# Kernel tuning notes

Measured on AMD Instinct MI355X. Metric: run time of the kernel, lower is better.

## Reference

```python
import jax, jax.numpy as jnp
import numpy as np

D_MODEL, H, D_K, D_V = 512, 8, 64, 64
S_Q, S_KV = 2048, 2048


def setup_inputs() -> dict:
    key = jax.random.key(0)
    ks = jax.random.split(key, 11)
    sc = 0.02
    return {
        "embeddings": jax.random.normal(ks[0], (S_Q, D_MODEL), jnp.float32),
        "K": jax.random.normal(ks[1], (S_KV, D_MODEL), jnp.float32),
        "V": jax.random.normal(ks[2], (S_KV, D_MODEL), jnp.float32),
        # per-head projection weights (stacked over heads) + biases
        "Wq": jax.random.normal(ks[3], (H, D_MODEL, D_K), jnp.float32) * sc,
        "bq": jax.random.normal(ks[4], (H, D_K), jnp.float32) * sc,
        "Wk": jax.random.normal(ks[5], (H, D_MODEL, D_K), jnp.float32) * sc,
        "bk": jax.random.normal(ks[6], (H, D_K), jnp.float32) * sc,
        "Wv": jax.random.normal(ks[7], (H, D_MODEL, D_V), jnp.float32) * sc,
        "bv": jax.random.normal(ks[8], (H, D_V), jnp.float32) * sc,
        # final linear: [h*d_v -> d_model]
        "Wo": jax.random.normal(ks[9], (H * D_V, D_MODEL), jnp.float32) * sc,
        "bo": jax.random.normal(ks[10], (D_MODEL,), jnp.float32) * sc,
    }


def reference(embeddings, K, V, Wq, bq, Wk, bk, Wv, bv, Wo, bo):
    # Batched per-head projections (the original loops over h heads; math identical)
    q = jnp.einsum("sd,hdk->hsk", embeddings, Wq) + bq[:, None, :]  # [h, Sq, d_k]
    k = jnp.einsum("td,hdk->htk", K, Wk) + bk[:, None, :]           # [h, Skv, d_k]
    v = jnp.einsum("td,hdv->htv", V, Wv) + bv[:, None, :]           # [h, Skv, d_v]
    scores = jnp.einsum("hsk,htk->hst", q, k) / jnp.sqrt(jnp.asarray(D_K, q.dtype))
    attn = jax.nn.softmax(scores, axis=-1)                           # [h, Sq, Skv]
    out = jnp.einsum("hst,htv->hsv", attn, v)                        # [h, Sq, d_v]
    # torch.cat(results, dim=1): head 0's d_v columns first -> [Sq, h*d_v]
    concat = jnp.transpose(out, (1, 0, 2)).reshape(S_Q, H * D_V)
    return concat @ Wo + bo                                          # [Sq, d_model]
```

## Files before the change

### kernel.cpp

```cpp
#include <hip/hip_runtime.h>

#define SQ 2048
#define DM 512
#define NH 8
#define NSPLIT 4

typedef __bf16 bf16x8 __attribute__((ext_vector_type(8)));
typedef float f32x4 __attribute__((ext_vector_type(4)));
typedef unsigned short us8 __attribute__((ext_vector_type(8)));

__device__ __forceinline__ unsigned short f2bf(float f) {
    unsigned u = __builtin_bit_cast(unsigned, f);
    u += 0x7fffu + ((u >> 16) & 1u);
    return (unsigned short)(u >> 16);
}
__device__ __forceinline__ float bf2f(unsigned short u) {
    return __builtin_bit_cast(float, (unsigned)u << 16);
}

__global__ __launch_bounds__(256) void convert_all(
    const float* __restrict__ emb, const float* __restrict__ Kin, const float* __restrict__ Vin,
    const float* __restrict__ Wq,  const float* __restrict__ Wk,  const float* __restrict__ Wv,
    const float* __restrict__ Wo,
    unsigned short* __restrict__ xe, unsigned short* __restrict__ xk, unsigned short* __restrict__ xv,
    unsigned short* __restrict__ Wt,
    unsigned short* __restrict__ Woth, unsigned short* __restrict__ Wotl)
{
    const int b = blockIdx.x, tid = threadIdx.x;
    __shared__ float ld[64 * 68];
    float4* ld4 = reinterpret_cast<float4*>(ld);

    if (b < 1536) {
        const int m = b >> 9;
        const float* src = (m == 0) ? emb : (m == 1) ? Kin : Vin;
        unsigned short* dst = (m == 0) ? xe : (m == 1) ? xk : xv;
        const int oct = (b & 511) * 256 + tid;
        const float4* s4 = reinterpret_cast<const float4*>(src + (size_t)oct * 8);
        float4 f0 = s4[0], f1 = s4[1];
        us8 o;
        o[0] = f2bf(f0.x); o[1] = f2bf(f0.y); o[2] = f2bf(f0.z); o[3] = f2bf(f0.w);
        o[4] = f2bf(f1.x); o[5] = f2bf(f1.y); o[6] = f2bf(f1.z); o[7] = f2bf(f1.w);
        *reinterpret_cast<us8*>(dst + (size_t)oct * 8) = o;
    } else if (b < 1728) {
        const int wi = b - 1536;
        const int idx = wi >> 3;
        const int kt = wi & 7;
        const int p = idx >> 3, h = idx & 7;
        const float* src = ((p == 0) ? Wq : (p == 1) ? Wk : Wv)
                         + (size_t)h * 512 * 64 + (size_t)kt * 64 * 64;
        unsigned short* dst = Wt + (size_t)idx * 64 * 512 + kt * 64;
        const int rr = tid >> 4, c4 = tid & 15;
        #pragma unroll
        for (int it = 0; it < 4; it++) {
            int r = rr + 16 * it;
            ld4[r * 17 + c4] = reinterpret_cast<const float4*>(src + (size_t)r * 64)[c4];
        }
        __syncthreads();
        #pragma unroll
        for (int it = 0; it < 2; it++) {
            int slot = tid + it * 256;
            int n = slot >> 3, g = slot & 7;
            us8 o;
            #pragma unroll
            for (int i = 0; i < 8; i++)
                o[i] = f2bf(ld[(g * 8 + i) * 68 + n]);
            *reinterpret_cast<us8*>(dst + (size_t)n * 512 + g * 8) = o;
        }
    } else {
        const int ti = b - 1728;
        const int kt = ti >> 3, nt = ti & 7;
        const float* src = Wo + (size_t)kt * 64 * 512 + nt * 64;
        const int rr = tid >> 4, c4 = tid & 15;
        #pragma unroll
        for (int it = 0; it < 4; it++) {
            int r = rr + 16 * it;
            ld4[r * 17 + c4] = reinterpret_cast<const float4*>(src + (size_t)r * 512)[c4];
        }
        __syncthreads();
        #pragma unroll
        for (int it = 0; it < 2; it++) {
            int slot = tid + it * 256;
            int n = slot >> 3, g = slot & 7;
            us8 oh, ol;
            #pragma unroll
            for (int i = 0; i < 8; i++) {
                float v = ld[(g * 8 + i) * 68 + n];
                unsigned short hi = f2bf(v);
                oh[i] = hi;
                ol[i] = f2bf(v - bf2f(hi));
            }
            size_t doff = (size_t)(nt * 64 + n) * 512 + kt * 64 + g * 8;
            *reinterpret_cast<us8*>(Woth + doff) = oh;
            *reinterpret_cast<us8*>(Wotl + doff) = ol;
        }
    }
}

__global__ __launch_bounds__(256) void qkv_mfma(
    const unsigned short* __restrict__ xe, const unsigned short* __restrict__ xk,
    const unsigned short* __restrict__ xv, const unsigned short* __restrict__ Wt,
    const float* __restrict__ bq, const float* __restrict__ bk, const float* __restrict__ bv,
    unsigned short* __restrict__ qo, unsigned short* __restrict__ ko, unsigned short* __restrict__ vo)
{
    const int p = blockIdx.z, h = blockIdx.y, s0 = blockIdx.x * 64;
    const unsigned short* X = (p == 0) ? xe : (p == 1) ? xk : xv;
    const unsigned short* W = Wt + (size_t)(p * 8 + h) * 64 * 512;
    const float* B = ((p == 0) ? bq : (p == 1) ? bk : bv) + h * 64;

    const int tid = threadIdx.x;
    const int w = tid >> 6, lane = tid & 63, cl = lane & 15, q4 = lane >> 4;
    const int sr = tid >> 3, sg = tid & 7;

    __shared__ unsigned short As[2][64 * 72];
    __shared__ unsigned short Bs[2][64 * 72];

    #pragma unroll
    for (int it = 0; it < 2; it++) {
        int r = sr + 32 * it;
        *reinterpret_cast<float4*>(&As[0][r * 72 + sg * 8]) =
            *reinterpret_cast<const float4*>(&X[(size_t)(s0 + r) * 512 + sg * 8]);
        *reinterpret_cast<float4*>(&Bs[0][r * 72 + sg * 8]) =
            *reinterpret_cast<const float4*>(&W[(size_t)r * 512 + sg * 8]);
    }

    f32x4 acc[4] = {};

    for (int c = 0; c < 8; c++) {
        __syncthreads();
        const int buf = c & 1;
        const bool more = (c + 1 < 8);
        float4 ar[2], br[2];
        if (more) {
            #pragma unroll
            for (int it = 0; it < 2; it++) {
                int r = sr + 32 * it;
                ar[it] = *reinterpret_cast<const float4*>(
                    &X[(size_t)(s0 + r) * 512 + (c + 1) * 64 + sg * 8]);
                br[it] = *reinterpret_cast<const float4*>(
                    &W[(size_t)r * 512 + (c + 1) * 64 + sg * 8]);
            }
        }

        bf16x8 a0 = *reinterpret_cast<const bf16x8*>(&As[buf][(16 * w + cl) * 72 + q4 * 8]);
        bf16x8 a1 = *reinterpret_cast<const bf16x8*>(&As[buf][(16 * w + cl) * 72 + 32 + q4 * 8]);
        #pragma unroll
        for (int nn = 0; nn < 4; nn++) {
            bf16x8 b0 = *reinterpret_cast<const bf16x8*>(&Bs[buf][(16 * nn + cl) * 72 + q4 * 8]);
            bf16x8 b1 = *reinterpret_cast<const bf16x8*>(&Bs[buf][(16 * nn + cl) * 72 + 32 + q4 * 8]);
            acc[nn] = __builtin_amdgcn_mfma_f32_16x16x32_bf16(a0, b0, acc[nn], 0, 0, 0);
            acc[nn] = __builtin_amdgcn_mfma_f32_16x16x32_bf16(a1, b1, acc[nn], 0, 0, 0);
        }

        if (more) {
            const int nbuf = buf ^ 1;
            #pragma unroll
            for (int it = 0; it < 2; it++) {
                int r = sr + 32 * it;
                *reinterpret_cast<float4*>(&As[nbuf][r * 72 + sg * 8]) = ar[it];
                *reinterpret_cast<float4*>(&Bs[nbuf][r * 72 + sg * 8]) = br[it];
            }
        }
    }

    if (p == 0) {
        #pragma unroll
        for (int nn = 0; nn < 4; nn++) {
            int col = 16 * nn + cl;
            float bb = B[col];
            #pragma unroll
            for (int r = 0; r < 4; r++)
                qo[((size_t)h * SQ + s0 + 16 * w + q4 * 4 + r) * 64 + col] =
                    f2bf((acc[nn][r] + bb) * 0.125f);
        }
    } else if (p == 1) {
        #pragma unroll
        for (int nn = 0; nn < 4; nn++) {
            int col = 16 * nn + cl;
            float bb = B[col];
            #pragma unroll
            for (int r = 0; r < 4; r++)
                ko[((size_t)h * SQ + s0 + 16 * w + q4 * 4 + r) * 64 + col] =
                    f2bf(acc[nn][r] + bb);
        }
    } else {
        #pragma unroll
        for (int nn = 0; nn < 4; nn++) {
            int col = 16 * nn + cl;
            float bb = B[col];
            ushort4 o;
            o.x = f2bf(acc[nn][0] + bb);
            o.y = f2bf(acc[nn][1] + bb);
            o.z = f2bf(acc[nn][2] + bb);
            o.w = f2bf(acc[nn][3] + bb);
            *reinterpret_cast<ushort4*>(
                vo + ((size_t)h * 64 + col) * SQ + s0 + 16 * w + q4 * 4) = o;
        }
    }
}

#define PW 72

__global__ __launch_bounds__(256) void attn_fwd(
    const unsigned short* __restrict__ qbf,
    const unsigned short* __restrict__ kbf,
    const unsigned short* __restrict__ vbf,
    float* __restrict__ Opart,
    float* __restrict__ lpart)
{
    const int h = blockIdx.y, s0 = blockIdx.x * 64, z = blockIdx.z;
    const int tid = threadIdx.x;
    const int w = tid >> 6, lane = tid & 63, cl = lane & 15, q4 = lane >> 4;
    const int NT = SQ / 64 / NSPLIT;
    const int t0 = z * NT;

    __shared__ unsigned short Ks[2][64 * PW];
    __shared__ unsigned short Vs[2][64 * PW];
    __shared__ unsigned short Ps[4][16 * PW];

    bf16x8 aq0 = *reinterpret_cast<const bf16x8*>(
        &qbf[((size_t)h * SQ + s0 + 16 * w + cl) * 64 + q4 * 8]);
    bf16x8 aq1 = *reinterpret_cast<const bf16x8*>(
        &qbf[((size_t)h * SQ + s0 + 16 * w + cl) * 64 + 32 + q4 * 8]);

    const int sr = tid >> 3, sg = tid & 7;

    #pragma unroll
    for (int it = 0; it < 2; it++) {
        int r = sr + 32 * it;
        *reinterpret_cast<float4*>(&Ks[0][r * PW + sg * 8]) =
            *reinterpret_cast<const float4*>(&kbf[((size_t)h * SQ + t0 * 64 + r) * 64 + sg * 8]);
        *reinterpret_cast<float4*>(&Vs[0][r * PW + sg * 8]) =
            *reinterpret_cast<const float4*>(&vbf[((size_t)h * 64 + r) * SQ + t0 * 64 + sg * 8]);
    }

    f32x4 o_acc[4] = {};
    float lsum[4] = {};

    for (int tl = 0; tl < NT; tl++) {
        __syncthreads();
        const int buf = tl & 1;
        const bool more = (tl + 1 < NT);
        float4 kr[2], vr[2];
        if (more) {
            #pragma unroll
            for (int it = 0; it < 2; it++) {
                int r = sr + 32 * it;
                kr[it] = *reinterpret_cast<const float4*>(
                    &kbf[((size_t)h * SQ + (t0 + tl + 1) * 64 + r) * 64 + sg * 8]);
                vr[it] = *reinterpret_cast<const float4*>(
                    &vbf[((size_t)h * 64 + r) * SQ + (t0 + tl + 1) * 64 + sg * 8]);
            }
        }

        f32x4 s_acc[4] = {};
        #pragma unroll
        for (int nn = 0; nn < 4; nn++) {
            bf16x8 b0 = *reinterpret_cast<const bf16x8*>(&Ks[buf][(16 * nn + cl) * PW + q4 * 8]);
            bf16x8 b1 = *reinterpret_cast<const bf16x8*>(&Ks[buf][(16 * nn + cl) * PW + 32 + q4 * 8]);
            s_acc[nn] = __builtin_amdgcn_mfma_f32_16x16x32_bf16(aq0, b0, s_acc[nn], 0, 0, 0);
            s_acc[nn] = __builtin_amdgcn_mfma_f32_16x16x32_bf16(aq1, b1, s_acc[nn], 0, 0, 0);
        }

        #pragma unroll
        for (int r = 0; r < 4; r++) {
            #pragma unroll
            for (int nn = 0; nn < 4; nn++) {
                float pv = __expf(s_acc[nn][r]);
                lsum[r] += pv;
                Ps[w][(q4 * 4 + r) * PW + 16 * nn + cl] = f2bf(pv);
            }
        }
        bf16x8 ap0 = *reinterpret_cast<const bf16x8*>(&Ps[w][cl * PW + q4 * 8]);
        bf16x8 ap1 = *reinterpret_cast<const bf16x8*>(&Ps[w][cl * PW + 32 + q4 * 8]);

        #pragma unroll
        for (int nn = 0; nn < 4; nn++) {
            bf16x8 b0 = *reinterpret_cast<const bf16x8*>(&Vs[buf][(16 * nn + cl) * PW + q4 * 8]);
            bf16x8 b1 = *reinterpret_cast<const bf16x8*>(&Vs[buf][(16 * nn + cl) * PW + 32 + q4 * 8]);
            o_acc[nn] = __builtin_amdgcn_mfma_f32_16x16x32_bf16(ap0, b0, o_acc[nn], 0, 0, 0);
            o_acc[nn] = __builtin_amdgcn_mfma_f32_16x16x32_bf16(ap1, b1, o_acc[nn], 0, 0, 0);
        }

        if (more) {
            const int nbuf = buf ^ 1;
            #pragma unroll
            for (int it = 0; it < 2; it++) {
                int r = sr + 32 * it;
                *reinterpret_cast<float4*>(&Ks[nbuf][r * PW + sg * 8]) = kr[it];
                *reinterpret_cast<float4*>(&Vs[nbuf][r * PW + sg * 8]) = vr[it];
            }
        }
    }

    #pragma unroll
    for (int r = 0; r < 4; r++) {
        float v = lsum[r];
        #pragma unroll
        for (int off = 1; off < 16; off <<= 1) v += __shfl_xor(v, off);
        lsum[r] = v;
    }

    const size_t zb = (size_t)(z * NH + h);
    if (cl == 0) {
        #pragma unroll
        for (int r = 0; r < 4; r++)
            lpart[zb * SQ + s0 + 16 * w + q4 * 4 + r] = lsum[r];
    }
    #pragma unroll
    for (int nn = 0; nn < 4; nn++)
        #pragma unroll
        for (int r = 0; r < 4; r++)
            Opart[(zb * SQ + s0 + 16 * w + q4 * 4 + r) * 64 + 16 * nn + cl] = o_acc[nn][r];
}

__global__ __launch_bounds__(256) void attn_combine(
    const float* __restrict__ Opart, const float* __restrict__ lpart,
    unsigned short* __restrict__ athi, unsigned short* __restrict__ atlo)
{
    const int gid = blockIdx.x * 256 + threadIdx.x;
    const int s = gid >> 6, oct = gid & 63;
    const int col0 = oct * 8, h = col0 >> 6, dv0 = col0 & 63;

    float l = 0.f;
    #pragma unroll
    for (int z = 0; z < NSPLIT; z++)
        l += lpart[(size_t)(z * NH + h) * SQ + s];
    const float inv = 1.0f / l;

    float o[8] = {};
    #pragma unroll
    for (int z = 0; z < NSPLIT; z++) {
        const float4* base = reinterpret_cast<const float4*>(
            Opart + ((size_t)(z * NH + h) * SQ + s) * 64 + dv0);
        float4 a = base[0], bq = base[1];
        o[0] += a.x; o[1] += a.y; o[2] += a.z; o[3] += a.w;
        o[4] += bq.x; o[5] += bq.y; o[6] += bq.z; o[7] += bq.w;
    }
    us8 hi, lo;
    #pragma unroll
    for (int i = 0; i < 8; i++) {
        float v = o[i] * inv;
        unsigned short hb = f2bf(v);
        hi[i] = hb;
        lo[i] = f2bf(v - bf2f(hb));
    }
    *reinterpret_cast<us8*>(athi + (size_t)s * DM + col0) = hi;
    *reinterpret_cast<us8*>(atlo + (size_t)s * DM + col0) = lo;
}

__global__ __launch_bounds__(256) void out_proj(
    const unsigned short* __restrict__ ah, const unsigned short* __restrict__ al,
    const unsigned short* __restrict__ Wh, const unsigned short* __restrict__ Wl,
    const float* __restrict__ bo, float* __restrict__ out)
{
    const int s0 = blockIdx.x * 64, n0 = blockIdx.y * 64;
    const int tid = threadIdx.x;
    const int w = tid >> 6, lane = tid & 63, cl = lane & 15, q4 = lane >> 4;
    const int sr = tid >> 3, sg = tid & 7;

    __shared__ unsigned short Ah[2][64 * 72], Al[2][64 * 72];
    __shared__ unsigned short Bh[2][64 * 72], Bl[2][64 * 72];

    #pragma unroll
    for (int it = 0; it < 2; it++) {
        int r = sr + 32 * it;
        *reinterpret_cast<float4*>(&Ah[0][r * 72 + sg * 8]) =
            *reinterpret_cast<const float4*>(&ah[(size_t)(s0 + r) * 512 + sg * 8]);
        *reinterpret_cast<float4*>(&Al[0][r * 72 + sg * 8]) =
            *reinterpret_cast<const float4*>(&al[(size_t)(s0 + r) * 512 + sg * 8]);
        *reinterpret_cast<float4*>(&Bh[0][r * 72 + sg * 8]) =
            *reinterpret_cast<const float4*>(&Wh[(size_t)(n0 + r) * 512 + sg * 8]);
        *reinterpret_cast<float4*>(&Bl[0][r * 72 + sg * 8]) =
            *reinterpret_cast<const float4*>(&Wl[(size_t)(n0 + r) * 512 + sg * 8]);
    }

    f32x4 acc[4] = {};

    for (int c = 0; c < 8; c++) {
        __syncthreads();
        const int buf = c & 1;
        const bool more = (c + 1 < 8);
        float4 ahr[2], alr[2], bhr[2], blr[2];
        if (more) {
            #pragma unroll
            for (int it = 0; it < 2; it++) {
                int r = sr + 32 * it;
                int off = (c + 1) * 64 + sg * 8;
                ahr[it] = *reinterpret_cast<const float4*>(&ah[(size_t)(s0 + r) * 512 + off]);
                alr[it] = *reinterpret_cast<const float4*>(&al[(size_t)(s0 + r) * 512 + off]);
                bhr[it] = *reinterpret_cast<const float4*>(&Wh[(size_t)(n0 + r) * 512 + off]);
                blr[it] = *reinterpret_cast<const float4*>(&Wl[(size_t)(n0 + r) * 512 + off]);
            }
        }

        bf16x8 ah0 = *reinterpret_cast<const bf16x8*>(&Ah[buf][(16 * w + cl) * 72 + q4 * 8]);
        bf16x8 ah1 = *reinterpret_cast<const bf16x8*>(&Ah[buf][(16 * w + cl) * 72 + 32 + q4 * 8]);
        bf16x8 al0 = *reinterpret_cast<const bf16x8*>(&Al[buf][(16 * w + cl) * 72 + q4 * 8]);
        bf16x8 al1 = *reinterpret_cast<const bf16x8*>(&Al[buf][(16 * w + cl) * 72 + 32 + q4 * 8]);
        #pragma unroll
        for (int nn = 0; nn < 4; nn++) {
            bf16x8 bh0 = *reinterpret_cast<const bf16x8*>(&Bh[buf][(16 * nn + cl) * 72 + q4 * 8]);
            bf16x8 bh1 = *reinterpret_cast<const bf16x8*>(&Bh[buf][(16 * nn + cl) * 72 + 32 + q4 * 8]);
            bf16x8 bl0 = *reinterpret_cast<const bf16x8*>(&Bl[buf][(16 * nn + cl) * 72 + q4 * 8]);
            bf16x8 bl1 = *reinterpret_cast<const bf16x8*>(&Bl[buf][(16 * nn + cl) * 72 + 32 + q4 * 8]);
            acc[nn] = __builtin_amdgcn_mfma_f32_16x16x32_bf16(ah0, bh0, acc[nn], 0, 0, 0);
            acc[nn] = __builtin_amdgcn_mfma_f32_16x16x32_bf16(ah1, bh1, acc[nn], 0, 0, 0);
            acc[nn] = __builtin_amdgcn_mfma_f32_16x16x32_bf16(ah0, bl0, acc[nn], 0, 0, 0);
            acc[nn] = __builtin_amdgcn_mfma_f32_16x16x32_bf16(ah1, bl1, acc[nn], 0, 0, 0);
            acc[nn] = __builtin_amdgcn_mfma_f32_16x16x32_bf16(al0, bh0, acc[nn], 0, 0, 0);
            acc[nn] = __builtin_amdgcn_mfma_f32_16x16x32_bf16(al1, bh1, acc[nn], 0, 0, 0);
        }

        if (more) {
            const int nbuf = buf ^ 1;
            #pragma unroll
            for (int it = 0; it < 2; it++) {
                int r = sr + 32 * it;
                *reinterpret_cast<float4*>(&Ah[nbuf][r * 72 + sg * 8]) = ahr[it];
                *reinterpret_cast<float4*>(&Al[nbuf][r * 72 + sg * 8]) = alr[it];
                *reinterpret_cast<float4*>(&Bh[nbuf][r * 72 + sg * 8]) = bhr[it];
                *reinterpret_cast<float4*>(&Bl[nbuf][r * 72 + sg * 8]) = blr[it];
            }
        }
    }

    #pragma unroll
    for (int nn = 0; nn < 4; nn++) {
        int col = n0 + 16 * nn + cl;
        float bb = bo[col];
        #pragma unroll
        for (int r = 0; r < 4; r++)
            out[(size_t)(s0 + 16 * w + q4 * 4 + r) * DM + col] = acc[nn][r] + bb;
    }
}

extern "C" void kernel_launch(void* const* d_in, const int* in_sizes, int n_in,
                              void* d_out, int out_size, void* d_ws, size_t ws_size,
                              hipStream_t stream) {
    const float* emb = (const float*)d_in[0];
    const float* Kin = (const float*)d_in[1];
    const float* Vin = (const float*)d_in[2];
    const float* Wq  = (const float*)d_in[3];
    const float* bq  = (const float*)d_in[4];
    const float* Wk  = (const float*)d_in[5];
    const float* bk  = (const float*)d_in[6];
    const float* Wv  = (const float*)d_in[7];
    const float* bv  = (const float*)d_in[8];
    const float* Wo  = (const float*)d_in[9];
    const float* bo  = (const float*)d_in[10];
    float* out = (float*)d_out;

    unsigned short* p = (unsigned short*)d_ws;
    unsigned short* xe   = p; p += (size_t)SQ * DM;
    unsigned short* xk   = p; p += (size_t)SQ * DM;
    unsigned short* xv   = p; p += (size_t)SQ * DM;
    unsigned short* Wt   = p; p += (size_t)24 * 64 * 512;
    unsigned short* Woth = p; p += (size_t)512 * 512;
    unsigned short* Wotl = p; p += (size_t)512 * 512;
    unsigned short* qbf  = p; p += (size_t)NH * SQ * 64;
    unsigned short* kbf  = p; p += (size_t)NH * SQ * 64;
    unsigned short* vbf  = p; p += (size_t)NH * SQ * 64;
    unsigned short* athi = p; p += (size_t)SQ * DM;
    unsigned short* atlo = p; p += (size_t)SQ * DM;
    float* Opart = (float*)p;
    float* lpart = Opart + (size_t)NSPLIT * NH * SQ * 64;

    convert_all<<<1792, 256, 0, stream>>>(emb, Kin, Vin, Wq, Wk, Wv, Wo,
                                          xe, xk, xv, Wt, Woth, Wotl);
    qkv_mfma<<<dim3(32, 8, 3), 256, 0, stream>>>(xe, xk, xv, Wt, bq, bk, bv,
                                                 qbf, kbf, vbf);
    attn_fwd<<<dim3(32, 8, NSPLIT), 256, 0, stream>>>(qbf, kbf, vbf, Opart, lpart);
    attn_combine<<<512, 256, 0, stream>>>(Opart, lpart, athi, atlo);
    out_proj<<<dim3(32, 8), 256, 0, stream>>>(athi, atlo, Woth, Wotl, bo, out);
}
```

Baseline: 127.8 us.

## Fuse activation conversion into QKV GEMM and split-K combine into output projection

Removes the standalone fp32-to-bf16 conversion of embeddings/K/V and converts them on the fly inside the QKV GEMM loads. The attention split combine is folded into out_proj, which sums the partials and normalizes by 1/l before packing to bf16. The hi/lo split precision for the output projection is dropped to a single bf16 pass, which reduces MFMA work by a factor of three. The attention grid is remapped and P uses truncating bf16 conversion. These changes cut kernel launches and intermediate traffic at the cost of lower numerical accuracy and redundant fp32 reads of the partials across the column blocks of out_proj.

```diff
diff --git a/kernel.cpp b/kernel.cpp
--- a/kernel.cpp
+++ b/kernel.cpp
@@ -14,42 +14,27 @@
     u += 0x7fffu + ((u >> 16) & 1u);
     return (unsigned short)(u >> 16);
 }
-__device__ __forceinline__ float bf2f(unsigned short u) {
-    return __builtin_bit_cast(float, (unsigned)u << 16);
-}
-
-__global__ __launch_bounds__(256) void convert_all(
-    const float* __restrict__ emb, const float* __restrict__ Kin, const float* __restrict__ Vin,
-    const float* __restrict__ Wq,  const float* __restrict__ Wk,  const float* __restrict__ Wv,
+__device__ __forceinline__ unsigned short f2bf_trunc(float f) {
+    return (unsigned short)(__builtin_bit_cast(unsigned, f) >> 16);
+}
+
+__global__ __launch_bounds__(256) void convert_w(
+    const float* __restrict__ Wq, const float* __restrict__ Wk, const float* __restrict__ Wv,
     const float* __restrict__ Wo,
-    unsigned short* __restrict__ xe, unsigned short* __restrict__ xk, unsigned short* __restrict__ xv,
-    unsigned short* __restrict__ Wt,
-    unsigned short* __restrict__ Woth, unsigned short* __restrict__ Wotl)
+    unsigned short* __restrict__ Wt, unsigned short* __restrict__ Wot)
 {
     const int b = blockIdx.x, tid = threadIdx.x;
     __shared__ float ld[64 * 68];
     float4* ld4 = reinterpret_cast<float4*>(ld);
-
-    if (b < 1536) {
-        const int m = b >> 9;
-        const float* src = (m == 0) ? emb : (m == 1) ? Kin : Vin;
-        unsigned short* dst = (m == 0) ? xe : (m == 1) ? xk : xv;
-        const int oct = (b & 511) * 256 + tid;
-        const float4* s4 = reinterpret_cast<const float4*>(src + (size_t)oct * 8);
-        float4 f0 = s4[0], f1 = s4[1];
-        us8 o;
-        o[0] = f2bf(f0.x); o[1] = f2bf(f0.y); o[2] = f2bf(f0.z); o[3] = f2bf(f0.w);
-        o[4] = f2bf(f1.x); o[5] = f2bf(f1.y); o[6] = f2bf(f1.z); o[7] = f2bf(f1.w);
-        *reinterpret_cast<us8*>(dst + (size_t)oct * 8) = o;
-    } else if (b < 1728) {
-        const int wi = b - 1536;
-        const int idx = wi >> 3;
-        const int kt = wi & 7;
+    const int rr = tid >> 4, c4 = tid & 15;
+
+    if (b < 192) {
+        const int idx = b >> 3;
+        const int kt = b & 7;
         const int p = idx >> 3, h = idx & 7;
         const float* src = ((p == 0) ? Wq : (p == 1) ? Wk : Wv)
                          + (size_t)h * 512 * 64 + (size_t)kt * 64 * 64;
         unsigned short* dst = Wt + (size_t)idx * 64 * 512 + kt * 64;
-        const int rr = tid >> 4, c4 = tid & 15;
         #pragma unroll
         for (int it = 0; it < 4; it++) {
             int r = rr + 16 * it;
@@ -67,10 +52,9 @@
             *reinterpret_cast<us8*>(dst + (size_t)n * 512 + g * 8) = o;
         }
     } else {
-        const int ti = b - 1728;
+        const int ti = b - 192;
         const int kt = ti >> 3, nt = ti & 7;
         const float* src = Wo + (size_t)kt * 64 * 512 + nt * 64;
-        const int rr = tid >> 4, c4 = tid & 15;
         #pragma unroll
         for (int it = 0; it < 4; it++) {
             int r = rr + 16 * it;
@@ -81,29 +65,23 @@
         for (int it = 0; it < 2; it++) {
             int slot = tid + it * 256;
             int n = slot >> 3, g = slot & 7;
-            us8 oh, ol;
-            #pragma unroll
-            for (int i = 0; i < 8; i++) {
-                float v = ld[(g * 8 + i) * 68 + n];
-                unsigned short hi = f2bf(v);
-                oh[i] = hi;
-                ol[i] = f2bf(v - bf2f(hi));
-            }
-            size_t doff = (size_t)(nt * 64 + n) * 512 + kt * 64 + g * 8;
-            *reinterpret_cast<us8*>(Woth + doff) = oh;
-            *reinterpret_cast<us8*>(Wotl + doff) = ol;
+            us8 o;
+            #pragma unroll
+            for (int i = 0; i < 8; i++)
+                o[i] = f2bf(ld[(g * 8 + i) * 68 + n]);
+            *reinterpret_cast<us8*>(Wot + (size_t)(nt * 64 + n) * 512 + kt * 64 + g * 8) = o;
         }
     }
 }
 
 __global__ __launch_bounds__(256) void qkv_mfma(
-    const unsigned short* __restrict__ xe, const unsigned short* __restrict__ xk,
-    const unsigned short* __restrict__ xv, const unsigned short* __restrict__ Wt,
+    const float* __restrict__ emb, const float* __restrict__ Kin, const float* __restrict__ Vin,
+    const unsigned short* __restrict__ Wt,
     const float* __restrict__ bq, const float* __restrict__ bk, const float* __restrict__ bv,
     unsigned short* __restrict__ qo, unsigned short* __restrict__ ko, unsigned short* __restrict__ vo)
 {
     const int p = blockIdx.z, h = blockIdx.y, s0 = blockIdx.x * 64;
-    const unsigned short* X = (p == 0) ? xe : (p == 1) ? xk : xv;
+    const float* X = (p == 0) ? emb : (p == 1) ? Kin : Vin;
     const unsigned short* W = Wt + (size_t)(p * 8 + h) * 64 * 512;
     const float* B = ((p == 0) ? bq : (p == 1) ? bk : bv) + h * 64;
 
@@ -117,8 +95,13 @@
     #pragma unroll
     for (int it = 0; it < 2; it++) {
         int r = sr + 32 * it;
-        *reinterpret_cast<float4*>(&As[0][r * 72 + sg * 8]) =
-            *reinterpret_cast<const float4*>(&X[(size_t)(s0 + r) * 512 + sg * 8]);
+        const float* xr = &X[(size_t)(s0 + r) * 512 + sg * 8];
+        float4 f0 = *reinterpret_cast<const float4*>(xr);
+        float4 f1 = *reinterpret_cast<const float4*>(xr + 4);
+        us8 o;
+        o[0] = f2bf(f0.x); o[1] = f2bf(f0.y); o[2] = f2bf(f0.z); o[3] = f2bf(f0.w);
+        o[4] = f2bf(f1.x); o[5] = f2bf(f1.y); o[6] = f2bf(f1.z); o[7] = f2bf(f1.w);
+        *reinterpret_cast<us8*>(&As[0][r * 72 + sg * 8]) = o;
         *reinterpret_cast<float4*>(&Bs[0][r * 72 + sg * 8]) =
             *reinterpret_cast<const float4*>(&W[(size_t)r * 512 + sg * 8]);
     }
@@ -129,13 +112,14 @@
         __syncthreads();
         const int buf = c & 1;
         const bool more = (c + 1 < 8);
-        float4 ar[2], br[2];
-        if (more) {
-            #pragma unroll
-            for (int it = 0; it < 2; it++) {
-                int r = sr + 32 * it;
-                ar[it] = *reinterpret_cast<const float4*>(
-                    &X[(size_t)(s0 + r) * 512 + (c + 1) * 64 + sg * 8]);
+        float4 x0[2], x1[2], br[2];
+        if (more) {
+            #pragma unroll
+            for (int it = 0; it < 2; it++) {
+                int r = sr + 32 * it;
+                const float* xr = &X[(size_t)(s0 + r) * 512 + (c + 1) * 64 + sg * 8];
+                x0[it] = *reinterpret_cast<const float4*>(xr);
+                x1[it] = *reinterpret_cast<const float4*>(xr + 4);
                 br[it] = *reinterpret_cast<const float4*>(
                     &W[(size_t)r * 512 + (c + 1) * 64 + sg * 8]);
             }
@@ -156,7 +140,12 @@
             #pragma unroll
             for (int it = 0; it < 2; it++) {
                 int r = sr + 32 * it;
-                *reinterpret_cast<float4*>(&As[nbuf][r * 72 + sg * 8]) = ar[it];
+                us8 o;
+                o[0] = f2bf(x0[it].x); o[1] = f2bf(x0[it].y);
+                o[2] = f2bf(x0[it].z); o[3] = f2bf(x0[it].w);
+                o[4] = f2bf(x1[it].x); o[5] = f2bf(x1[it].y);
+                o[6] = f2bf(x1[it].z); o[7] = f2bf(x1[it].w);
+                *reinterpret_cast<us8*>(&As[nbuf][r * 72 + sg * 8]) = o;
                 *reinterpret_cast<float4*>(&Bs[nbuf][r * 72 + sg * 8]) = br[it];
             }
         }
@@ -207,7 +196,9 @@
     float* __restrict__ Opart,
     float* __restrict__ lpart)
 {
-    const int h = blockIdx.y, s0 = blockIdx.x * 64, z = blockIdx.z;
+    const int bx = blockIdx.x;
+    const int z = bx >> 3, h = bx & 7;
+    const int s0 = blockIdx.y * 64;
     const int tid = threadIdx.x;
     const int w = tid >> 6, lane = tid & 63, cl = lane & 15, q4 = lane >> 4;
     const int NT = SQ / 64 / NSPLIT;
@@ -267,7 +258,7 @@
             for (int nn = 0; nn < 4; nn++) {
                 float pv = __expf(s_acc[nn][r]);
                 lsum[r] += pv;
-                Ps[w][(q4 * 4 + r) * PW + 16 * nn + cl] = f2bf(pv);
+                Ps[w][(q4 * 4 + r) * PW + 16 * nn + cl] = f2bf_trunc(pv);
             }
         }
         bf16x8 ap0 = *reinterpret_cast<const bf16x8*>(&Ps[w][cl * PW + q4 * 8]);
@@ -300,7 +291,7 @@
         lsum[r] = v;
     }
 
-    const size_t zb = (size_t)(z * NH + h);
+    const size_t zb = (size_t)bx;
     if (cl == 0) {
         #pragma unroll
         for (int r = 0; r < 4; r++)
@@ -313,44 +304,9 @@
             Opart[(zb * SQ + s0 + 16 * w + q4 * 4 + r) * 64 + 16 * nn + cl] = o_acc[nn][r];
 }
 
-__global__ __launch_bounds__(256) void attn_combine(
+__global__ __launch_bounds__(256) void out_proj(
     const float* __restrict__ Opart, const float* __restrict__ lpart,
-    unsigned short* __restrict__ athi, unsigned short* __restrict__ atlo)
-{
-    const int gid = blockIdx.x * 256 + threadIdx.x;
-    const int s = gid >> 6, oct = gid & 63;
-    const int col0 = oct * 8, h = col0 >> 6, dv0 = col0 & 63;
-
-    float l = 0.f;
-    #pragma unroll
-    for (int z = 0; z < NSPLIT; z++)
-        l += lpart[(size_t)(z * NH + h) * SQ + s];
-    const float inv = 1.0f / l;
-
-    float o[8] = {};
-    #pragma unroll
-    for (int z = 0; z < NSPLIT; z++) {
-        const float4* base = reinterpret_cast<const float4*>(
-            Opart + ((size_t)(z * NH + h) * SQ + s) * 64 + dv0);
-        float4 a = base[0], bq = base[1];
-        o[0] += a.x; o[1] += a.y; o[2] += a.z; o[3] += a.w;
-        o[4] += bq.x; o[5] += bq.y; o[6] += bq.z; o[7] += bq.w;
-    }
-    us8 hi, lo;
-    #pragma unroll
-    for (int i = 0; i < 8; i++) {
-        float v = o[i] * inv;
-        unsigned short hb = f2bf(v);
-        hi[i] = hb;
-        lo[i] = f2bf(v - bf2f(hb));
-    }
-    *reinterpret_cast<us8*>(athi + (size_t)s * DM + col0) = hi;
-    *reinterpret_cast<us8*>(atlo + (size_t)s * DM + col0) = lo;
-}
-
-__global__ __launch_bounds__(256) void out_proj(
-    const unsigned short* __restrict__ ah, const unsigned short* __restrict__ al,
-    const unsigned short* __restrict__ Wh, const unsigned short* __restrict__ Wl,
+    const unsigned short* __restrict__ Wot,
     const float* __restrict__ bo, float* __restrict__ out)
 {
     const int s0 = blockIdx.x * 64, n0 = blockIdx.y * 64;
@@ -358,20 +314,41 @@
     const int w = tid >> 6, lane = tid & 63, cl = lane & 15, q4 = lane >> 4;
     const int sr = tid >> 3, sg = tid & 7;
 
-    __shared__ unsigned short Ah[2][64 * 72], Al[2][64 * 72];
-    __shared__ unsigned short Bh[2][64 * 72], Bl[2][64 * 72];
+    __shared__ unsigned short As[2][64 * 72];
+    __shared__ unsigned short Bs[2][64 * 72];
+    __shared__ float invL[512];
+
+    #pragma unroll
+    for (int k = 0; k < 2; k++) {
+        int idx = tid * 2 + k;
+        int hh = idx >> 6, ss = idx & 63;
+        float l = 0.f;
+        #pragma unroll
+        for (int z = 0; z < NSPLIT; z++)
+            l += lpart[(size_t)(z * 8 + hh) * SQ + s0 + ss];
+        invL[idx] = 1.0f / l;
+    }
+    __syncthreads();
 
     #pragma unroll
     for (int it = 0; it < 2; it++) {
         int r = sr + 32 * it;
-        *reinterpret_cast<float4*>(&Ah[0][r * 72 + sg * 8]) =
-            *reinterpret_cast<const float4*>(&ah[(size_t)(s0 + r) * 512 + sg * 8]);
-        *reinterpret_cast<float4*>(&Al[0][r * 72 + sg * 8]) =
-            *reinterpret_cast<const float4*>(&al[(size_t)(s0 + r) * 512 + sg * 8]);
-        *reinterpret_cast<float4*>(&Bh[0][r * 72 + sg * 8]) =
-            *reinterpret_cast<const float4*>(&Wh[(size_t)(n0 + r) * 512 + sg * 8]);
-        *reinterpret_cast<float4*>(&Bl[0][r * 72 + sg * 8]) =
-            *reinterpret_cast<const float4*>(&Wl[(size_t)(n0 + r) * 512 + sg * 8]);
+        float o[8] = {};
+        #pragma unroll
+        for (int z = 0; z < NSPLIT; z++) {
+            const float4* pp = reinterpret_cast<const float4*>(
+                &Opart[((size_t)(z * 8) * SQ + s0 + r) * 64 + sg * 8]);
+            float4 a = pp[0], b = pp[1];
+            o[0] += a.x; o[1] += a.y; o[2] += a.z; o[3] += a.w;
+            o[4] += b.x; o[5] += b.y; o[6] += b.z; o[7] += b.w;
+        }
+        float il = invL[r];
+        us8 pk;
+        #pragma unroll
+        for (int i = 0; i < 8; i++) pk[i] = f2bf(o[i] * il);
+        *reinterpret_cast<us8*>(&As[0][r * 72 + sg * 8]) = pk;
+        *reinterpret_cast<float4*>(&Bs[0][r * 72 + sg * 8]) =
+            *reinterpret_cast<const float4*>(&Wot[(size_t)(n0 + r) * 512 + sg * 8]);
     }
 
     f32x4 acc[4] = {};
@@ -380,46 +357,54 @@
         __syncthreads();
         const int buf = c & 1;
         const bool more = (c + 1 < 8);
-        float4 ahr[2], alr[2], bhr[2], blr[2];
-        if (more) {
-            #pragma unroll
-            for (int it = 0; it < 2; it++) {
-                int r = sr + 32 * it;
-                int off = (c + 1) * 64 + sg * 8;
-                ahr[it] = *reinterpret_cast<const float4*>(&ah[(size_t)(s0 + r) * 512 + off]);
-                alr[it] = *reinterpret_cast<const float4*>(&al[(size_t)(s0 + r) * 512 + off]);
-                bhr[it] = *reinterpret_cast<const float4*>(&Wh[(size_t)(n0 + r) * 512 + off]);
-                blr[it] = *reinterpret_cast<const float4*>(&Wl[(size_t)(n0 + r) * 512 + off]);
-            }
-        }
-
-        bf16x8 ah0 = *reinterpret_cast<const bf16x8*>(&Ah[buf][(16 * w + cl) * 72 + q4 * 8]);
-        bf16x8 ah1 = *reinterpret_cast<const bf16x8*>(&Ah[buf][(16 * w + cl) * 72 + 32 + q4 * 8]);
-        bf16x8 al0 = *reinterpret_cast<const bf16x8*>(&Al[buf][(16 * w + cl) * 72 + q4 * 8]);
-        bf16x8 al1 = *reinterpret_cast<const bf16x8*>(&Al[buf][(16 * w + cl) * 72 + 32 + q4 * 8]);
-        #pragma unroll
-        for (int nn = 0; nn < 4; nn++) {
-            bf16x8 bh0 = *reinterpret_cast<const bf16x8*>(&Bh[buf][(16 * nn + cl) * 72 + q4 * 8]);
-            bf16x8 bh1 = *reinterpret_cast<const bf16x8*>(&Bh[buf][(16 * nn + cl) * 72 + 32 + q4 * 8]);
-            bf16x8 bl0 = *reinterpret_cast<const bf16x8*>(&Bl[buf][(16 * nn + cl) * 72 + q4 * 8]);
-            bf16x8 bl1 = *reinterpret_cast<const bf16x8*>(&Bl[buf][(16 * nn + cl) * 72 + 32 + q4 * 8]);
-            acc[nn] = __builtin_amdgcn_mfma_f32_16x16x32_bf16(ah0, bh0, acc[nn], 0, 0, 0);
-            acc[nn] = __builtin_amdgcn_mfma_f32_16x16x32_bf16(ah1, bh1, acc[nn], 0, 0, 0);
-            acc[nn] = __builtin_amdgcn_mfma_f32_16x16x32_bf16(ah0, bl0, acc[nn], 0, 0, 0);
-            acc[nn] = __builtin_amdgcn_mfma_f32_16x16x32_bf16(ah1, bl1, acc[nn], 0, 0, 0);
-            acc[nn] = __builtin_amdgcn_mfma_f32_16x16x32_bf16(al0, bh0, acc[nn], 0, 0, 0);
-            acc[nn] = __builtin_amdgcn_mfma_f32_16x16x32_bf16(al1, bh1, acc[nn], 0, 0, 0);
+        float4 pre[2][NSPLIT][2];
+        float4 wr[2];
+        if (more) {
+            const int hn = c + 1;
+            #pragma unroll
+            for (int it = 0; it < 2; it++) {
+                int r = sr + 32 * it;
+                #pragma unroll
+                for (int z = 0; z < NSPLIT; z++) {
+                    const float4* pp = reinterpret_cast<const float4*>(
+                        &Opart[((size_t)(z * 8 + hn) * SQ + s0 + r) * 64 + sg * 8]);
+                    pre[it][z][0] = pp[0];
+                    pre[it][z][1] = pp[1];
+                }
+                wr[it] = *reinterpret_cast<const float4*>(
+                    &Wot[(size_t)(n0 + r) * 512 + hn * 64 + sg * 8]);
+            }
+        }
+
+        bf16x8 a0 = *reinterpret_cast<const bf16x8*>(&As[buf][(16 * w + cl) * 72 + q4 * 8]);
+        bf16x8 a1 = *reinterpret_cast<const bf16x8*>(&As[buf][(16 * w + cl) * 72 + 32 + q4 * 8]);
+        #pragma unroll
+        for (int nn = 0; nn < 4; nn++) {
+            bf16x8 b0 = *reinterpret_cast<const bf16x8*>(&Bs[buf][(16 * nn + cl) * 72 + q4 * 8]);
+            bf16x8 b1 = *reinterpret_cast<const bf16x8*>(&Bs[buf][(16 * nn + cl) * 72 + 32 + q4 * 8]);
+            acc[nn] = __builtin_amdgcn_mfma_f32_16x16x32_bf16(a0, b0, acc[nn], 0, 0, 0);
+            acc[nn] = __builtin_amdgcn_mfma_f32_16x16x32_bf16(a1, b1, acc[nn], 0, 0, 0);
         }
 
         if (more) {
             const int nbuf = buf ^ 1;
-            #pragma unroll
-            for (int it = 0; it < 2; it++) {
-                int r = sr + 32 * it;
-                *reinterpret_cast<float4*>(&Ah[nbuf][r * 72 + sg * 8]) = ahr[it];
-                *reinterpret_cast<float4*>(&Al[nbuf][r * 72 + sg * 8]) = alr[it];
-                *reinterpret_cast<float4*>(&Bh[nbuf][r * 72 + sg * 8]) = bhr[it];
-                *reinterpret_cast<float4*>(&Bl[nbuf][r * 72 + sg * 8]) = blr[it];
+            const int hn = c + 1;
+            #pragma unroll
+            for (int it = 0; it < 2; it++) {
+                int r = sr + 32 * it;
+                float o[8] = {};
+                #pragma unroll
+                for (int z = 0; z < NSPLIT; z++) {
+                    float4 a = pre[it][z][0], b = pre[it][z][1];
+                    o[0] += a.x; o[1] += a.y; o[2] += a.z; o[3] += a.w;
+                    o[4] += b.x; o[5] += b.y; o[6] += b.z; o[7] += b.w;
+                }
+                float il = invL[hn * 64 + r];
+                us8 pk;
+                #pragma unroll
+                for (int i = 0; i < 8; i++) pk[i] = f2bf(o[i] * il);
+                *reinterpret_cast<us8*>(&As[nbuf][r * 72 + sg * 8]) = pk;
+                *reinterpret_cast<float4*>(&Bs[nbuf][r * 72 + sg * 8]) = wr[it];
             }
         }
     }
@@ -451,25 +436,17 @@
     float* out = (float*)d_out;
 
     unsigned short* p = (unsigned short*)d_ws;
-    unsigned short* xe   = p; p += (size_t)SQ * DM;
-    unsigned short* xk   = p; p += (size_t)SQ * DM;
-    unsigned short* xv   = p; p += (size_t)SQ * DM;
-    unsigned short* Wt   = p; p += (size_t)24 * 64 * 512;
-    unsigned short* Woth = p; p += (size_t)512 * 512;
-    unsigned short* Wotl = p; p += (size_t)512 * 512;
-    unsigned short* qbf  = p; p += (size_t)NH * SQ * 64;
-    unsigned short* kbf  = p; p += (size_t)NH * SQ * 64;
-    unsigned short* vbf  = p; p += (size_t)NH * SQ * 64;
-    unsigned short* athi = p; p += (size_t)SQ * DM;
-    unsigned short* atlo = p; p += (size_t)SQ * DM;
+    unsigned short* Wt  = p; p += (size_t)24 * 64 * 512;
+    unsigned short* Wot = p; p += (size_t)512 * 512;
+    unsigned short* qbf = p; p += (size_t)NH * SQ * 64;
+    unsigned short* kbf = p; p += (size_t)NH * SQ * 64;
+    unsigned short* vbf = p; p += (size_t)NH * SQ * 64;
     float* Opart = (float*)p;
     float* lpart = Opart + (size_t)NSPLIT * NH * SQ * 64;
 
-    convert_all<<<1792, 256, 0, stream>>>(emb, Kin, Vin, Wq, Wk, Wv, Wo,
-                                          xe, xk, xv, Wt, Woth, Wotl);
-    qkv_mfma<<<dim3(32, 8, 3), 256, 0, stream>>>(xe, xk, xv, Wt, bq, bk, bv,
+    convert_w<<<256, 256, 0, stream>>>(Wq, Wk, Wv, Wo, Wt, Wot);
+    qkv_mfma<<<dim3(32, 8, 3), 256, 0, stream>>>(emb, Kin, Vin, Wt, bq, bk, bv,
                                                  qbf, kbf, vbf);
-    attn_fwd<<<dim3(32, 8, NSPLIT), 256, 0, stream>>>(qbf, kbf, vbf, Opart, lpart);
-    attn_combine<<<512, 256, 0, stream>>>(Opart, lpart, athi, atlo);
-    out_proj<<<dim3(32, 8), 256, 0, stream>>>(athi, atlo, Woth, Wotl, bo, out);
-}
+    attn_fwd<<<dim3(32, 32), 256, 0, stream>>>(qbf, kbf, vbf, Opart, lpart);
+    out_proj<<<dim3(32, 8), 256, 0, stream>>>(Opart, lpart, Wot, bo, out);
+}
```

Result: slower. 130.6 us (+2.2%).
